# Optimization experiments

Hardware: AMD Instinct MI355X
Metric: run time of the kernel (lower is better)

The kernel has to match this reference:

```python
import jax, jax.numpy as jnp
import numpy as np

EPS = 0.1

def _kernels():
    # torch: sobel = [[-0.5,0,0.5]]*3 (2D), repeated along depth -> [1,1,3,3,3]
    s = np.array([[-0.5, 0.0, 0.5]] * 3, dtype=np.float32)        # grad along W
    kx = np.tile(s[None, :, :], (3, 1, 1))                        # [3,3,3]
    ky = np.tile(s.T[None, :, :], (3, 1, 1))                      # grad along H
    kz = np.zeros((3, 3, 3), dtype=np.float32)
    kz[0, :, :] = -0.5
    kz[2, :, :] = 0.5                                             # grad along D
    # OIDHW, O=I=1 (channel=1 depthwise)
    return (jnp.asarray(kx)[None, None], jnp.asarray(ky)[None, None], jnp.asarray(kz)[None, None])

KX, KY, KZ = _kernels()

def _conv(x, k):
    return jax.lax.conv_general_dilated(
        x, k, window_strides=(1, 1, 1), padding='VALID',
        dimension_numbers=('NCDHW', 'OIDHW', 'NCDHW'))

def _grads(x):
    # ReplicationPad3d(1) == edge padding on D,H,W
    xp = jnp.pad(x, ((0, 0), (0, 0), (1, 1), (1, 1), (1, 1)), mode='edge')
    return _conv(xp, KX), _conv(xp, KY), _conv(xp, KZ)

def setup_inputs() -> dict:
    key = jax.random.key(0)
    k1, k2, k3 = jax.random.split(key, 3)
    shp = (1, 1, 192, 192, 192)
    return {
        'I': jax.random.normal(k1, shp, dtype=jnp.float32),
        'J': jax.random.normal(k2, shp, dtype=jnp.float32),
        'mask': jax.random.uniform(k3, shp, dtype=jnp.float32),
    }

def reference(I, J, mask):
    Ix, Iy, Iz = _grads(I)
    Jx, Jy, Jz = _grads(J)
    I_mag = Ix * Ix + Iy * Iy + Iz * Iz + EPS * EPS
    J_mag = Jx * Jx + Jy * Jy + Jz * Jz + EPS * EPS
    dot = Ix * Jx + Iy * Jy + Iz * Jz          # == sum over concat channel dim (C=1)
    ngf = (dot * dot) / (I_mag * J_mag)
    return jnp.mean((1.0 - ngf) * mask)
```

## Files before the change

### kernel.cpp

```cpp
#include <hip/hip_runtime.h>

#define NN 192
#define YCHUNK 8
#define BZ 4

__device__ __forceinline__ void load_row(const float* __restrict__ row, int x0, float v[6]) {
    const float4 c = *reinterpret_cast<const float4*>(row + x0);
    v[1] = c.x; v[2] = c.y; v[3] = c.z; v[4] = c.w;
    v[0] = row[(x0 == 0) ? 0 : (x0 - 1)];
    v[5] = row[(x0 + 4 > NN - 1) ? (NN - 1) : (x0 + 4)];
}

__device__ __forceinline__ void load_slot(const float* __restrict__ A,
                                          int bm, int b0, int bp, int x0,
                                          float sa[4], float sb[4], float tb[4]) {
    float vm[6], v0[6], vp[6];
    load_row(A + bm, x0, vm);
    load_row(A + b0, x0, v0);
    load_row(A + bp, x0, vp);
#pragma unroll
    for (int i = 0; i < 4; ++i) {
        const float am = vm[i + 2] - vm[i];
        const float a0 = v0[i + 2] - v0[i];
        const float ap = vp[i + 2] - vp[i];
        const float bmv = vm[i] + vm[i + 1] + vm[i + 2];
        const float b0v = v0[i] + v0[i + 1] + v0[i + 2];
        const float bpv = vp[i] + vp[i + 1] + vp[i + 2];
        sa[i] = am + a0 + ap;
        sb[i] = bmv + b0v + bpv;
        tb[i] = bpv - bmv;
    }
}

__global__ __launch_bounds__(192) void ngf_kernel(const float* __restrict__ I,
                                                  const float* __restrict__ J,
                                                  const float* __restrict__ M,
                                                  float* __restrict__ out) {
    const int xg = threadIdx.x;
    const int x0 = xg * 4;
    const int z = blockIdx.y * BZ + threadIdx.y;
    const int ybase = blockIdx.x * YCHUNK;

    const int gzm = (z == 0) ? 0 : z - 1;
    const int gzp = (z == NN - 1) ? (NN - 1) : z + 1;
    const int zbm = gzm * NN, zb0 = z * NN, zbp = gzp * NN;

    float saI[3][4], sbI[3][4], tbI[3][4];
    float saJ[3][4], sbJ[3][4], tbJ[3][4];

    {
        const int gy = (ybase == 0) ? 0 : ybase - 1;
        load_slot(I, (zbm + gy) * NN, (zb0 + gy) * NN, (zbp + gy) * NN, x0,
                  saI[0], sbI[0], tbI[0]);
        load_slot(J, (zbm + gy) * NN, (zb0 + gy) * NN, (zbp + gy) * NN, x0,
                  saJ[0], sbJ[0], tbJ[0]);
        load_slot(I, (zbm + ybase) * NN, (zb0 + ybase) * NN, (zbp + ybase) * NN, x0,
                  saI[1], sbI[1], tbI[1]);
        load_slot(J, (zbm + ybase) * NN, (zb0 + ybase) * NN, (zbp + ybase) * NN, x0,
                  saJ[1], sbJ[1], tbJ[1]);
    }

    float acc = 0.0f;
#pragma unroll
    for (int yy = 0; yy < YCHUNK; ++yy) {
        const int y = ybase + yy;
        const int gyp = (y == NN - 1) ? (NN - 1) : y + 1;
        const int s0 = yy % 3, s1 = (yy + 1) % 3, s2 = (yy + 2) % 3;
        load_slot(I, (zbm + gyp) * NN, (zb0 + gyp) * NN, (zbp + gyp) * NN, x0,
                  saI[s2], sbI[s2], tbI[s2]);
        load_slot(J, (zbm + gyp) * NN, (zb0 + gyp) * NN, (zbp + gyp) * NN, x0,
                  saJ[s2], sbJ[s2], tbJ[s2]);
        const float4 m4 = *reinterpret_cast<const float4*>(M + (zb0 + y) * NN + x0);
        const float mm[4] = {m4.x, m4.y, m4.z, m4.w};
#pragma unroll
        for (int i = 0; i < 4; ++i) {
            const float Ix = saI[s0][i] + saI[s1][i] + saI[s2][i];
            const float Iy = sbI[s2][i] - sbI[s0][i];
            const float Iz = tbI[s0][i] + tbI[s1][i] + tbI[s2][i];
            const float Jx = saJ[s0][i] + saJ[s1][i] + saJ[s2][i];
            const float Jy = sbJ[s2][i] - sbJ[s0][i];
            const float Jz = tbJ[s0][i] + tbJ[s1][i] + tbJ[s2][i];
            const float imag = Ix * Ix + Iy * Iy + Iz * Iz + 0.04f;
            const float jmag = Jx * Jx + Jy * Jy + Jz * Jz + 0.04f;
            const float dot = Ix * Jx + Iy * Jy + Iz * Jz;
            const float ngf = (dot * dot) / (imag * jmag);
            acc += (1.0f - ngf) * mm[i];
        }
    }

    acc *= (1.0f / ((float)NN * (float)NN * (float)NN));
#pragma unroll
    for (int off = 32; off > 0; off >>= 1)
        acc += __shfl_down(acc, off, 64);

    __shared__ float red[3];
    const int flat = threadIdx.y * 48 + threadIdx.x;
    if ((flat & 63) == 0) red[flat >> 6] = acc;
    __syncthreads();
    if (flat == 0) atomicAdd(out, red[0] + red[1] + red[2]);
}

extern "C" void kernel_launch(void* const* d_in, const int* in_sizes, int n_in,
                              void* d_out, int out_size, void* d_ws, size_t ws_size,
                              hipStream_t stream) {
    const float* I = (const float*)d_in[0];
    const float* J = (const float*)d_in[1];
    const float* M = (const float*)d_in[2];
    float* out = (float*)d_out;

    hipMemsetAsync(d_out, 0, sizeof(float), stream);

    dim3 block(48, BZ);
    dim3 grid(NN / YCHUNK, NN / BZ);
    ngf_kernel<<<grid, block, 0, stream>>>(I, J, M, out);
}
```

Before: 131.7 us.

## Map one wavefront per row with 3 elements per lane and shuffle halos

Each wavefront now handles one full (z,y) row, with every lane computing 3 consecutive x outputs. The x-neighbour values come from wave shuffles instead of extra halo loads. The sliding y-window register reuse is dropped, so each output row loads all 9 neighbouring rows of I and J directly and relies on the cache for reuse across rows. The division is also replaced with a fast reciprocal intrinsic. This removes the scalar halo loads and the register pressure, at the cost of more redundant global and L2 traffic.

```diff
diff --git a/kernel.cpp b/kernel.cpp
--- a/kernel.cpp
+++ b/kernel.cpp
@@ -1,91 +1,74 @@
 #include <hip/hip_runtime.h>
 
 #define NN 192
-#define YCHUNK 8
-#define BZ 4
 
-__device__ __forceinline__ void load_row(const float* __restrict__ row, int x0, float v[6]) {
-    const float4 c = *reinterpret_cast<const float4*>(row + x0);
-    v[1] = c.x; v[2] = c.y; v[3] = c.z; v[4] = c.w;
-    v[0] = row[(x0 == 0) ? 0 : (x0 - 1)];
-    v[5] = row[(x0 + 4 > NN - 1) ? (NN - 1) : (x0 + 4)];
+
+__device__ __forceinline__ float3 ld3(const float* p) { return *(const float3*)p; }
+
+__device__ __forceinline__ void grads(const float* __restrict__ Ab,
+                                      const int zr[3], const int yo[3],
+                                      int lane, float G[3][3]) {
+    float p[3][3], q[3][3];
+#pragma unroll
+    for (int yy = 0; yy < 3; ++yy) {
+        const float3 a = ld3(Ab + zr[0] + yo[yy]);
+        const float3 b = ld3(Ab + zr[1] + yo[yy]);
+        const float3 c = ld3(Ab + zr[2] + yo[yy]);
+        p[yy][0] = a.x + b.x + c.x;  q[yy][0] = c.x - a.x;
+        p[yy][1] = a.y + b.y + c.y;  q[yy][1] = c.y - a.y;
+        p[yy][2] = a.z + b.z + c.z;  q[yy][2] = c.z - a.z;
+    }
+    float S[3], D[3], T[3];
+#pragma unroll
+    for (int i = 0; i < 3; ++i) {
+        S[i] = p[0][i] + p[1][i] + p[2][i];
+        D[i] = p[2][i] - p[0][i];
+        T[i] = q[0][i] + q[1][i] + q[2][i];
+    }
+    float SL = __shfl_up(S[2], 1, 64), SR = __shfl_down(S[0], 1, 64);
+    float DL = __shfl_up(D[2], 1, 64), DR = __shfl_down(D[0], 1, 64);
+    float TL = __shfl_up(T[2], 1, 64), TR = __shfl_down(T[0], 1, 64);
+    if (lane == 0)  { SL = S[0]; DL = D[0]; TL = T[0]; }
+    if (lane == 63) { SR = S[2]; DR = D[2]; TR = T[2]; }
+    G[0][0] = S[1] - SL;           G[0][1] = S[2] - S[0];        G[0][2] = SR - S[1];
+    G[1][0] = DL + D[0] + D[1];    G[1][1] = D[0] + D[1] + D[2]; G[1][2] = D[1] + D[2] + DR;
+    G[2][0] = TL + T[0] + T[1];    G[2][1] = T[0] + T[1] + T[2]; G[2][2] = T[1] + T[2] + TR;
 }
 
-__device__ __forceinline__ void load_slot(const float* __restrict__ A,
-                                          int bm, int b0, int bp, int x0,
-                                          float sa[4], float sb[4], float tb[4]) {
-    float vm[6], v0[6], vp[6];
-    load_row(A + bm, x0, vm);
-    load_row(A + b0, x0, v0);
-    load_row(A + bp, x0, vp);
-#pragma unroll
-    for (int i = 0; i < 4; ++i) {
-        const float am = vm[i + 2] - vm[i];
-        const float a0 = v0[i + 2] - v0[i];
-        const float ap = vp[i + 2] - vp[i];
-        const float bmv = vm[i] + vm[i + 1] + vm[i + 2];
-        const float b0v = v0[i] + v0[i + 1] + v0[i + 2];
-        const float bpv = vp[i] + vp[i + 1] + vp[i + 2];
-        sa[i] = am + a0 + ap;
-        sb[i] = bmv + b0v + bpv;
-        tb[i] = bpv - bmv;
-    }
-}
+__global__ __launch_bounds__(256, 4) void ngf_kernel(const float* __restrict__ I,
+                                                     const float* __restrict__ J,
+                                                     const float* __restrict__ M,
+                                                     float* __restrict__ out) {
+    const int lane = threadIdx.x;
+    const int wy = threadIdx.y;
+    const int z = blockIdx.y;
+    const int y = blockIdx.x * 4 + wy;
 
-__global__ __launch_bounds__(192) void ngf_kernel(const float* __restrict__ I,
-                                                  const float* __restrict__ J,
-                                                  const float* __restrict__ M,
-                                                  float* __restrict__ out) {
-    const int xg = threadIdx.x;
-    const int x0 = xg * 4;
-    const int z = blockIdx.y * BZ + threadIdx.y;
-    const int ybase = blockIdx.x * YCHUNK;
+    const int zm = (z == 0) ? 0 : z - 1;
+    const int zp = (z == NN - 1) ? (NN - 1) : z + 1;
+    const int ym = (y == 0) ? 0 : y - 1;
+    const int yp = (y == NN - 1) ? (NN - 1) : y + 1;
 
-    const int gzm = (z == 0) ? 0 : z - 1;
-    const int gzp = (z == NN - 1) ? (NN - 1) : z + 1;
-    const int zbm = gzm * NN, zb0 = z * NN, zbp = gzp * NN;
+    const int zr[3] = {zm * NN * NN, z * NN * NN, zp * NN * NN};
+    const int yo[3] = {ym * NN, y * NN, yp * NN};
 
-    float saI[3][4], sbI[3][4], tbI[3][4];
-    float saJ[3][4], sbJ[3][4], tbJ[3][4];
+    const int xoff = lane * 3;
+    const float3 m3 = ld3(M + zr[1] + yo[1] + xoff);
 
-    {
-        const int gy = (ybase == 0) ? 0 : ybase - 1;
-        load_slot(I, (zbm + gy) * NN, (zb0 + gy) * NN, (zbp + gy) * NN, x0,
-                  saI[0], sbI[0], tbI[0]);
-        load_slot(J, (zbm + gy) * NN, (zb0 + gy) * NN, (zbp + gy) * NN, x0,
-                  saJ[0], sbJ[0], tbJ[0]);
-        load_slot(I, (zbm + ybase) * NN, (zb0 + ybase) * NN, (zbp + ybase) * NN, x0,
-                  saI[1], sbI[1], tbI[1]);
-        load_slot(J, (zbm + ybase) * NN, (zb0 + ybase) * NN, (zbp + ybase) * NN, x0,
-                  saJ[1], sbJ[1], tbJ[1]);
-    }
+    float GI[3][3], GJ[3][3];
+    grads(I + xoff, zr, yo, lane, GI);
+    grads(J + xoff, zr, yo, lane, GJ);
 
+    const float mm[3] = {m3.x, m3.y, m3.z};
     float acc = 0.0f;
 #pragma unroll
-    for (int yy = 0; yy < YCHUNK; ++yy) {
-        const int y = ybase + yy;
-        const int gyp = (y == NN - 1) ? (NN - 1) : y + 1;
-        const int s0 = yy % 3, s1 = (yy + 1) % 3, s2 = (yy + 2) % 3;
-        load_slot(I, (zbm + gyp) * NN, (zb0 + gyp) * NN, (zbp + gyp) * NN, x0,
-                  saI[s2], sbI[s2], tbI[s2]);
-        load_slot(J, (zbm + gyp) * NN, (zb0 + gyp) * NN, (zbp + gyp) * NN, x0,
-                  saJ[s2], sbJ[s2], tbJ[s2]);
-        const float4 m4 = *reinterpret_cast<const float4*>(M + (zb0 + y) * NN + x0);
-        const float mm[4] = {m4.x, m4.y, m4.z, m4.w};
-#pragma unroll
-        for (int i = 0; i < 4; ++i) {
-            const float Ix = saI[s0][i] + saI[s1][i] + saI[s2][i];
-            const float Iy = sbI[s2][i] - sbI[s0][i];
-            const float Iz = tbI[s0][i] + tbI[s1][i] + tbI[s2][i];
-            const float Jx = saJ[s0][i] + saJ[s1][i] + saJ[s2][i];
-            const float Jy = sbJ[s2][i] - sbJ[s0][i];
-            const float Jz = tbJ[s0][i] + tbJ[s1][i] + tbJ[s2][i];
-            const float imag = Ix * Ix + Iy * Iy + Iz * Iz + 0.04f;
-            const float jmag = Jx * Jx + Jy * Jy + Jz * Jz + 0.04f;
-            const float dot = Ix * Jx + Iy * Jy + Iz * Jz;
-            const float ngf = (dot * dot) / (imag * jmag);
-            acc += (1.0f - ngf) * mm[i];
-        }
+    for (int i = 0; i < 3; ++i) {
+        const float Ix = GI[0][i], Iy = GI[1][i], Iz = GI[2][i];
+        const float Jx = GJ[0][i], Jy = GJ[1][i], Jz = GJ[2][i];
+        const float im = Ix * Ix + Iy * Iy + Iz * Iz + 0.04f;
+        const float jm = Jx * Jx + Jy * Jy + Jz * Jz + 0.04f;
+        const float dot = Ix * Jx + Iy * Jy + Iz * Jz;
+        acc += (1.0f - dot * dot * __builtin_amdgcn_rcpf(im * jm)) * mm[i];
     }
 
     acc *= (1.0f / ((float)NN * (float)NN * (float)NN));
@@ -93,11 +76,11 @@
     for (int off = 32; off > 0; off >>= 1)
         acc += __shfl_down(acc, off, 64);
 
-    __shared__ float red[3];
-    const int flat = threadIdx.y * 48 + threadIdx.x;
-    if ((flat & 63) == 0) red[flat >> 6] = acc;
+    __shared__ float red[4];
+    if (lane == 0) red[wy] = acc;
     __syncthreads();
-    if (flat == 0) atomicAdd(out, red[0] + red[1] + red[2]);
+    if (wy == 0 && lane == 0)
+        atomicAdd(out, (red[0] + red[1]) + (red[2] + red[3]));
 }
 
 extern "C" void kernel_launch(void* const* d_in, const int* in_sizes, int n_in,
@@ -110,7 +93,7 @@
 
     hipMemsetAsync(d_out, 0, sizeof(float), stream);
 
-    dim3 block(48, BZ);
-    dim3 grid(NN / YCHUNK, NN / BZ);
+    dim3 block(64, 4);
+    dim3 grid(NN / 4, NN);
     ngf_kernel<<<grid, block, 0, stream>>>(I, J, M, out);
 }
```

Measured after the change: 211.5 us. 60.7% more time.
